# Kernel optimization log

Hardware: AMD Instinct MI355X
Metric: run time of the kernel (lower is better)

The kernel has to match this reference:

```python
import jax, jax.numpy as jnp
import numpy as np
import math

B, H, N, D = 4, 8, 2048, 64


def setup_inputs() -> dict:
    key = jax.random.key(0)
    kq, kk, kv = jax.random.split(key, 3)
    q = jax.random.normal(kq, (B, H, N, D), dtype=jnp.float32)
    k = jax.random.normal(kk, (B, H, N, D), dtype=jnp.float32)
    v = jax.random.normal(kv, (B, H, N, D), dtype=jnp.float32)
    return {"q": q, "k": k, "v": v}


def reference(q, k, v):
    # global_attention_Sub: expanded squared L2 distance ||q_i - k_j||^2
    # = qq_i - 2 q_i.k_j + kk_j, then softmax(-dist/sqrt(D)) @ v.
    scale = math.sqrt(q.shape[-1])
    inner = -2.0 * jnp.einsum('bhnd,bhmd->bhnm', q, k)          # [B,H,N,N]
    qq = jnp.sum(q * q, axis=-1, keepdims=True)                  # [B,H,N,1]
    kk = jnp.sum(k * k, axis=-1, keepdims=True)                  # [B,H,N,1]
    diff_sq = qq + inner + jnp.swapaxes(kk, -1, -2)              # [B,H,N,N]
    attn = jax.nn.softmax(-diff_sq / scale, axis=-1)
    x = jnp.einsum('bhnm,bhmd->bhnd', attn, v)                   # [B,H,N,D]
    return jnp.transpose(x, (0, 2, 1, 3))                        # [B,N,H,D]
```

## Files before the change

kernel.cpp:

```cpp
#include <hip/hip_runtime.h>

typedef __bf16 bf16x4 __attribute__((ext_vector_type(4)));
typedef __bf16 bf16x8 __attribute__((ext_vector_type(8)));
typedef float floatx4 __attribute__((ext_vector_type(4)));

constexpr int Bc = 4, Hc = 8, Nc = 2048, Dc = 64;
constexpr int BQ = 128;
constexpr int WQ = 32;
constexpr int TK = 64;
constexpr int NT = Nc / TK;
constexpr int SPS = 72;
constexpr float LOG2E = 1.44269504088896340736f;

constexpr size_t KSW_OFF = 0;
constexpr size_t VSW_OFF = (size_t)32 * NT * 8192;
constexpr size_t KKN_OFF = VSW_OFF * 2;

typedef __attribute__((address_space(1))) const unsigned int gu32;
typedef __attribute__((address_space(3))) unsigned int lu32;
__device__ __forceinline__ void dma16(const void* g, void* l) {
    __builtin_amdgcn_global_load_lds((gu32*)g, (lu32*)l, 16, 0, 0);
}
__device__ __forceinline__ void dma4(const void* g, void* l) {
    __builtin_amdgcn_global_load_lds((gu32*)g, (lu32*)l, 4, 0, 0);
}

__global__ __launch_bounds__(256) void prep_kernel(
    const float* __restrict__ Kg, const float* __restrict__ Vg, char* __restrict__ ws)
{
    __shared__ float sT[64 * 68];
    const int tid = threadIdx.x;
    const int jt = blockIdx.x, bh = blockIdx.y;

    __bf16* Ksw = (__bf16*)(ws + KSW_OFF) + ((size_t)bh * NT + jt) * 4096;
    __bf16* Vsw = (__bf16*)(ws + VSW_OFF) + ((size_t)bh * NT + jt) * 4096;
    float*  kkn = (float*)(ws + KKN_OFF) + (size_t)bh * Nc + jt * 64;
    const size_t tb = ((size_t)bh * Nc + jt * 64) * Dc;

#pragma unroll
    for (int cc = 0; cc < 2; ++cc) {
        const int g   = tid + cc * 256;
        const int key = g >> 3, kcx = g & 7;
        const int kc  = kcx ^ (key & 7);
        const float* src = Kg + tb + key * 64 + kc * 8;
        float4 a = *(const float4*)src;
        float4 b = *(const float4*)(src + 4);
        float ss = a.x*a.x + a.y*a.y + a.z*a.z + a.w*a.w
                 + b.x*b.x + b.y*b.y + b.z*b.z + b.w*b.w;
        ss += __shfl_xor(ss, 1);
        ss += __shfl_xor(ss, 2);
        ss += __shfl_xor(ss, 4);
        if (kcx == 0) kkn[key] = -(ss * 0.125f * LOG2E);
        bf16x8 c8;
        c8[0]=(__bf16)a.x; c8[1]=(__bf16)a.y; c8[2]=(__bf16)a.z; c8[3]=(__bf16)a.w;
        c8[4]=(__bf16)b.x; c8[5]=(__bf16)b.y; c8[6]=(__bf16)b.z; c8[7]=(__bf16)b.w;
        *(bf16x8*)(Ksw + g * 8) = c8;
    }

    {
        const int js = tid >> 2, dc = (tid & 3) * 16;
        const float* vr = Vg + tb + js * 64 + dc;
        float* dst = &sT[js * 68 + dc];
        *(float4*)dst       = *(const float4*)vr;
        *(float4*)(dst + 4) = *(const float4*)(vr + 4);
        *(float4*)(dst + 8) = *(const float4*)(vr + 8);
        *(float4*)(dst + 12)= *(const float4*)(vr + 12);
    }
    __syncthreads();

#pragma unroll
    for (int cc = 0; cc < 2; ++cc) {
        const int g = tid + cc * 256;
        const int d = g >> 3, kcx = g & 7;
        const int kc = kcx ^ (d & 7);
        bf16x8 c8;
#pragma unroll
        for (int e = 0; e < 8; ++e) {
            const int ee = (e + kcx) & 7;
            c8[ee] = (__bf16)sT[(kc * 8 + ee) * 68 + d];
        }
        *(bf16x8*)(Vsw + g * 8) = c8;
    }
}

__global__ __launch_bounds__(256, 2) void attn_kernel(
    const float* __restrict__ Qg, const char* __restrict__ ws, float* __restrict__ Og)
{
    __shared__ __align__(16) __bf16 sK[2][4096];
    __shared__ __align__(16) __bf16 sV[2][4096];
    __shared__ __align__(16) float  skk[2][64];
    __shared__ __align__(16) __bf16 sP[BQ * SPS];
    __shared__ __align__(16) float  sl[BQ];

    const int tid  = threadIdx.x;
    const int wave = tid >> 6;
    const int lane = tid & 63;
    const int qd   = lane >> 4;
    const int c    = lane & 15;

    const int qt = blockIdx.x;
    const int bh = blockIdx.y;

    const char* Kimg = ws + KSW_OFF + (size_t)bh * NT * 8192;
    const char* Vimg = ws + VSW_OFF + (size_t)bh * NT * 8192;
    const float* kkp = (const float*)(ws + KKN_OFF) + (size_t)bh * Nc;

    const float qscale = 0.25f * LOG2E;
    const int i0 = qt * BQ + wave * WQ;

    bf16x8 qf[2][2];
#pragma unroll
    for (int h = 0; h < 2; ++h) {
        const float* qrow = Qg + ((size_t)bh * Nc + i0 + h * 16 + c) * Dc + qd * 8;
#pragma unroll
        for (int ks = 0; ks < 2; ++ks) {
            float4 a = *(const float4*)(qrow + ks * 32);
            float4 b = *(const float4*)(qrow + ks * 32 + 4);
            bf16x8 f;
            f[0] = (__bf16)(a.x * qscale); f[1] = (__bf16)(a.y * qscale);
            f[2] = (__bf16)(a.z * qscale); f[3] = (__bf16)(a.w * qscale);
            f[4] = (__bf16)(b.x * qscale); f[5] = (__bf16)(b.y * qscale);
            f[6] = (__bf16)(b.z * qscale); f[7] = (__bf16)(b.w * qscale);
            qf[h][ks] = f;
        }
    }

    const int koff0 = c * 64 + ((qd ^ (c & 7)) << 3);
    const int koff1 = c * 64 + (((4 + qd) ^ (c & 7)) << 3);

    floatx4 oacc[2][4];
#pragma unroll
    for (int h = 0; h < 2; ++h)
#pragma unroll
        for (int dt = 0; dt < 4; ++dt)
#pragma unroll
            for (int e = 0; e < 4; ++e) oacc[h][dt][e] = 0.f;
    float lp[2] = {0.f, 0.f};

    auto stage = [&](int jt2, int b) {
        const char* ki = Kimg + (size_t)jt2 * 8192;
        const char* vi = Vimg + (size_t)jt2 * 8192;
#pragma unroll
        for (int i = 0; i < 2; ++i) {
            const int off    = wave * 2048 + i * 1024 + lane * 16;
            const int ldsoff = wave * 2048 + i * 1024;
            dma16(ki + off, (char*)&sK[b][0] + ldsoff);
            dma16(vi + off, (char*)&sV[b][0] + ldsoff);
        }
        if (wave == 3) dma4(kkp + jt2 * 64 + lane, &skk[b][0]);
    };

    stage(0, 0);

    for (int jt = 0; jt < NT; ++jt) {
        const int b = jt & 1;
        __syncthreads();
        if (jt + 1 < NT) stage(jt + 1, b ^ 1);

        floatx4 st[2][4];
#pragma unroll
        for (int kt = 0; kt < 4; ++kt) {
            floatx4 kkf = *(const floatx4*)&skk[b][kt * 16 + qd * 4];
            st[0][kt] = kkf; st[1][kt] = kkf;
        }
#pragma unroll
        for (int kt = 0; kt < 4; ++kt) {
            const __bf16* kbase = &sK[b][kt * 1024];
            bf16x8 kf0 = *(const bf16x8*)(kbase + koff0);
            bf16x8 kf1 = *(const bf16x8*)(kbase + koff1);
            st[0][kt] = __builtin_amdgcn_mfma_f32_16x16x32_bf16(kf0, qf[0][0], st[0][kt], 0, 0, 0);
            st[0][kt] = __builtin_amdgcn_mfma_f32_16x16x32_bf16(kf1, qf[0][1], st[0][kt], 0, 0, 0);
            st[1][kt] = __builtin_amdgcn_mfma_f32_16x16x32_bf16(kf0, qf[1][0], st[1][kt], 0, 0, 0);
            st[1][kt] = __builtin_amdgcn_mfma_f32_16x16x32_bf16(kf1, qf[1][1], st[1][kt], 0, 0, 0);
        }

#pragma unroll
        for (int h = 0; h < 2; ++h) {
            const int prow = wave * WQ + h * 16 + c;
#pragma unroll
            for (int kt = 0; kt < 4; ++kt) {
                float p0 = __builtin_amdgcn_exp2f(st[h][kt][0]);
                float p1 = __builtin_amdgcn_exp2f(st[h][kt][1]);
                float p2 = __builtin_amdgcn_exp2f(st[h][kt][2]);
                float p3 = __builtin_amdgcn_exp2f(st[h][kt][3]);
                lp[h] += (p0 + p1) + (p2 + p3);
                bf16x4 pk;
                pk[0] = (__bf16)p0; pk[1] = (__bf16)p1;
                pk[2] = (__bf16)p2; pk[3] = (__bf16)p3;
                *(bf16x4*)&sP[prow * SPS + kt * 16 + qd * 4] = pk;
            }
        }
        bf16x8 pf[2][2];
#pragma unroll
        for (int h = 0; h < 2; ++h)
#pragma unroll
            for (int ks = 0; ks < 2; ++ks)
                pf[h][ks] = *(const bf16x8*)&sP[(wave * WQ + h * 16 + c) * SPS + ks * 32 + qd * 8];

#pragma unroll
        for (int dt = 0; dt < 4; ++dt) {
            const __bf16* vbase = &sV[b][dt * 1024];
            bf16x8 vf0 = *(const bf16x8*)(vbase + koff0);
            bf16x8 vf1 = *(const bf16x8*)(vbase + koff1);
            oacc[0][dt] = __builtin_amdgcn_mfma_f32_16x16x32_bf16(pf[0][0], vf0, oacc[0][dt], 0, 0, 0);
            oacc[0][dt] = __builtin_amdgcn_mfma_f32_16x16x32_bf16(pf[0][1], vf1, oacc[0][dt], 0, 0, 0);
            oacc[1][dt] = __builtin_amdgcn_mfma_f32_16x16x32_bf16(pf[1][0], vf0, oacc[1][dt], 0, 0, 0);
            oacc[1][dt] = __builtin_amdgcn_mfma_f32_16x16x32_bf16(pf[1][1], vf1, oacc[1][dt], 0, 0, 0);
        }
    }

#pragma unroll
    for (int h = 0; h < 2; ++h) {
        float l = lp[h];
        l += __shfl_xor(l, 16);
        l += __shfl_xor(l, 32);
        if (qd == 0) sl[wave * WQ + h * 16 + c] = l;
    }
    const int b_ = bh >> 3, hh = bh & 7;
#pragma unroll
    for (int h = 0; h < 2; ++h) {
        floatx4 lf = *(const floatx4*)&sl[wave * WQ + h * 16 + qd * 4];
#pragma unroll
        for (int r = 0; r < 4; ++r) {
            const float inv = 1.f / lf[r];
            const int i = i0 + h * 16 + qd * 4 + r;
            float* orow = Og + (((size_t)b_ * Nc + i) * Hc + hh) * Dc + c;
#pragma unroll
            for (int dt = 0; dt < 4; ++dt)
                orow[dt * 16] = oacc[h][dt][r] * inv;
        }
    }
}

extern "C" void kernel_launch(void* const* d_in, const int* in_sizes, int n_in,
                              void* d_out, int out_size, void* d_ws, size_t ws_size,
                              hipStream_t stream) {
    const float* q = (const float*)d_in[0];
    const float* k = (const float*)d_in[1];
    const float* v = (const float*)d_in[2];
    float* out = (float*)d_out;
    char* ws = (char*)d_ws;
    prep_kernel<<<dim3(NT, Bc * Hc), 256, 0, stream>>>(k, v, ws);
    attn_kernel<<<dim3(Nc / BQ, Bc * Hc), 256, 0, stream>>>(q, ws, out);
}
```

Before: 140.8 us.

## Split key tile across wave pairs, each wave owning 64 query rows

Reorganizes the attention block so that each wave handles 64 query rows and half of each 64-key tile (a 2x2 split of query halves and key halves), instead of 32 query rows over all keys. Each K and V fragment read from LDS now feeds four MFMAs instead of two, which reduces LDS read traffic per MFMA, and the P scratch becomes per-wave with a smaller stride. In exchange, the accumulators double in register footprint (16 floatx4 for the output plus Q fragments), which may hurt occupancy at launch_bounds(256,2). It also adds a cross-wave reduction epilogue through a new LDS buffer, with extra barriers, to merge the two key-half partial outputs and row sums.

```diff
diff --git a/kernel.cpp b/kernel.cpp
--- a/kernel.cpp
+++ b/kernel.cpp
@@ -6,10 +6,9 @@
 
 constexpr int Bc = 4, Hc = 8, Nc = 2048, Dc = 64;
 constexpr int BQ = 128;
-constexpr int WQ = 32;
 constexpr int TK = 64;
 constexpr int NT = Nc / TK;
-constexpr int SPS = 72;
+constexpr int SPS = 40;
 constexpr float LOG2E = 1.44269504088896340736f;
 
 constexpr size_t KSW_OFF = 0;
@@ -56,7 +55,6 @@
         c8[4]=(__bf16)b.x; c8[5]=(__bf16)b.y; c8[6]=(__bf16)b.z; c8[7]=(__bf16)b.w;
         *(bf16x8*)(Ksw + g * 8) = c8;
     }
-
     {
         const int js = tid >> 2, dc = (tid & 3) * 16;
         const float* vr = Vg + tb + js * 64 + dc;
@@ -67,7 +65,6 @@
         *(float4*)(dst + 12)= *(const float4*)(vr + 12);
     }
     __syncthreads();
-
 #pragma unroll
     for (int cc = 0; cc < 2; ++cc) {
         const int g = tid + cc * 256;
@@ -89,14 +86,17 @@
     __shared__ __align__(16) __bf16 sK[2][4096];
     __shared__ __align__(16) __bf16 sV[2][4096];
     __shared__ __align__(16) float  skk[2][64];
-    __shared__ __align__(16) __bf16 sP[BQ * SPS];
-    __shared__ __align__(16) float  sl[BQ];
+    __shared__ __align__(16) __bf16 sP[4][64 * SPS];
+    __shared__ __align__(16) float  sl[256];
+    __shared__ __align__(16) float  sO[64 * 68];
 
     const int tid  = threadIdx.x;
     const int wave = tid >> 6;
     const int lane = tid & 63;
     const int qd   = lane >> 4;
     const int c    = lane & 15;
+    const int kh   = wave >> 1;
+    const int qh   = wave & 1;
 
     const int qt = blockIdx.x;
     const int bh = blockIdx.y;
@@ -106,12 +106,12 @@
     const float* kkp = (const float*)(ws + KKN_OFF) + (size_t)bh * Nc;
 
     const float qscale = 0.25f * LOG2E;
-    const int i0 = qt * BQ + wave * WQ;
-
-    bf16x8 qf[2][2];
-#pragma unroll
-    for (int h = 0; h < 2; ++h) {
-        const float* qrow = Qg + ((size_t)bh * Nc + i0 + h * 16 + c) * Dc + qd * 8;
+    const int i0 = qt * BQ + qh * 64;
+
+    bf16x8 qf[4][2];
+#pragma unroll
+    for (int h4 = 0; h4 < 4; ++h4) {
+        const float* qrow = Qg + ((size_t)bh * Nc + i0 + h4 * 16 + c) * Dc + qd * 8;
 #pragma unroll
         for (int ks = 0; ks < 2; ++ks) {
             float4 a = *(const float4*)(qrow + ks * 32);
@@ -121,114 +121,138 @@
             f[2] = (__bf16)(a.z * qscale); f[3] = (__bf16)(a.w * qscale);
             f[4] = (__bf16)(b.x * qscale); f[5] = (__bf16)(b.y * qscale);
             f[6] = (__bf16)(b.z * qscale); f[7] = (__bf16)(b.w * qscale);
-            qf[h][ks] = f;
-        }
-    }
-
-    const int koff0 = c * 64 + ((qd ^ (c & 7)) << 3);
-    const int koff1 = c * 64 + (((4 + qd) ^ (c & 7)) << 3);
-
-    floatx4 oacc[2][4];
-#pragma unroll
-    for (int h = 0; h < 2; ++h)
+            qf[h4][ks] = f;
+        }
+    }
+
+    int koffK[2][2], voff[4];
+#pragma unroll
+    for (int kt = 0; kt < 2; ++kt)
+#pragma unroll
+        for (int ks = 0; ks < 2; ++ks) {
+            const int key = kh * 32 + kt * 16 + c;
+            koffK[kt][ks] = key * 64 + (((ks * 4 + qd) ^ (key & 7)) << 3);
+        }
+#pragma unroll
+    for (int dt = 0; dt < 4; ++dt) {
+        const int d = dt * 16 + c;
+        voff[dt] = d * 64 + (((kh * 4 + qd) ^ (d & 7)) << 3);
+    }
+
+    floatx4 oacc[4][4];
+#pragma unroll
+    for (int h4 = 0; h4 < 4; ++h4)
 #pragma unroll
         for (int dt = 0; dt < 4; ++dt)
 #pragma unroll
-            for (int e = 0; e < 4; ++e) oacc[h][dt][e] = 0.f;
-    float lp[2] = {0.f, 0.f};
+            for (int e = 0; e < 4; ++e) oacc[h4][dt][e] = 0.f;
+    float lp[4] = {0.f, 0.f, 0.f, 0.f};
 
     auto stage = [&](int jt2, int b) {
         const char* ki = Kimg + (size_t)jt2 * 8192;
         const char* vi = Vimg + (size_t)jt2 * 8192;
 #pragma unroll
         for (int i = 0; i < 2; ++i) {
-            const int off    = wave * 2048 + i * 1024 + lane * 16;
-            const int ldsoff = wave * 2048 + i * 1024;
-            dma16(ki + off, (char*)&sK[b][0] + ldsoff);
-            dma16(vi + off, (char*)&sV[b][0] + ldsoff);
+            const int off = wave * 2048 + i * 1024;
+            dma16(ki + off + lane * 16, (char*)&sK[b][0] + off);
+            dma16(vi + off + lane * 16, (char*)&sV[b][0] + off);
         }
         if (wave == 3) dma4(kkp + jt2 * 64 + lane, &skk[b][0]);
     };
 
     stage(0, 0);
+
+    __bf16* sPw = &sP[wave][0];
 
     for (int jt = 0; jt < NT; ++jt) {
         const int b = jt & 1;
         __syncthreads();
         if (jt + 1 < NT) stage(jt + 1, b ^ 1);
 
-        floatx4 st[2][4];
-#pragma unroll
-        for (int kt = 0; kt < 4; ++kt) {
-            floatx4 kkf = *(const floatx4*)&skk[b][kt * 16 + qd * 4];
-            st[0][kt] = kkf; st[1][kt] = kkf;
-        }
-#pragma unroll
-        for (int kt = 0; kt < 4; ++kt) {
-            const __bf16* kbase = &sK[b][kt * 1024];
-            bf16x8 kf0 = *(const bf16x8*)(kbase + koff0);
-            bf16x8 kf1 = *(const bf16x8*)(kbase + koff1);
-            st[0][kt] = __builtin_amdgcn_mfma_f32_16x16x32_bf16(kf0, qf[0][0], st[0][kt], 0, 0, 0);
-            st[0][kt] = __builtin_amdgcn_mfma_f32_16x16x32_bf16(kf1, qf[0][1], st[0][kt], 0, 0, 0);
-            st[1][kt] = __builtin_amdgcn_mfma_f32_16x16x32_bf16(kf0, qf[1][0], st[1][kt], 0, 0, 0);
-            st[1][kt] = __builtin_amdgcn_mfma_f32_16x16x32_bf16(kf1, qf[1][1], st[1][kt], 0, 0, 0);
-        }
-
-#pragma unroll
-        for (int h = 0; h < 2; ++h) {
-            const int prow = wave * WQ + h * 16 + c;
-#pragma unroll
-            for (int kt = 0; kt < 4; ++kt) {
-                float p0 = __builtin_amdgcn_exp2f(st[h][kt][0]);
-                float p1 = __builtin_amdgcn_exp2f(st[h][kt][1]);
-                float p2 = __builtin_amdgcn_exp2f(st[h][kt][2]);
-                float p3 = __builtin_amdgcn_exp2f(st[h][kt][3]);
-                lp[h] += (p0 + p1) + (p2 + p3);
+#pragma unroll
+        for (int kt = 0; kt < 2; ++kt) {
+            floatx4 kkf = *(const floatx4*)&skk[b][kh * 32 + kt * 16 + qd * 4];
+            floatx4 st[4];
+#pragma unroll
+            for (int h4 = 0; h4 < 4; ++h4) st[h4] = kkf;
+#pragma unroll
+            for (int ks = 0; ks < 2; ++ks) {
+                bf16x8 kf = *(const bf16x8*)(&sK[b][0] + koffK[kt][ks]);
+                st[0] = __builtin_amdgcn_mfma_f32_16x16x32_bf16(kf, qf[0][ks], st[0], 0, 0, 0);
+                st[1] = __builtin_amdgcn_mfma_f32_16x16x32_bf16(kf, qf[1][ks], st[1], 0, 0, 0);
+                st[2] = __builtin_amdgcn_mfma_f32_16x16x32_bf16(kf, qf[2][ks], st[2], 0, 0, 0);
+                st[3] = __builtin_amdgcn_mfma_f32_16x16x32_bf16(kf, qf[3][ks], st[3], 0, 0, 0);
+            }
+#pragma unroll
+            for (int h4 = 0; h4 < 4; ++h4) {
+                float p0 = __builtin_amdgcn_exp2f(st[h4][0]);
+                float p1 = __builtin_amdgcn_exp2f(st[h4][1]);
+                float p2 = __builtin_amdgcn_exp2f(st[h4][2]);
+                float p3 = __builtin_amdgcn_exp2f(st[h4][3]);
+                lp[h4] += (p0 + p1) + (p2 + p3);
                 bf16x4 pk;
                 pk[0] = (__bf16)p0; pk[1] = (__bf16)p1;
                 pk[2] = (__bf16)p2; pk[3] = (__bf16)p3;
-                *(bf16x4*)&sP[prow * SPS + kt * 16 + qd * 4] = pk;
+                *(bf16x4*)&sPw[(h4 * 16 + c) * SPS + kt * 16 + qd * 4] = pk;
             }
         }
-        bf16x8 pf[2][2];
-#pragma unroll
-        for (int h = 0; h < 2; ++h)
-#pragma unroll
-            for (int ks = 0; ks < 2; ++ks)
-                pf[h][ks] = *(const bf16x8*)&sP[(wave * WQ + h * 16 + c) * SPS + ks * 32 + qd * 8];
+
+        bf16x8 pf[4];
+#pragma unroll
+        for (int h4 = 0; h4 < 4; ++h4)
+            pf[h4] = *(const bf16x8*)&sPw[(h4 * 16 + c) * SPS + qd * 8];
 
 #pragma unroll
         for (int dt = 0; dt < 4; ++dt) {
-            const __bf16* vbase = &sV[b][dt * 1024];
-            bf16x8 vf0 = *(const bf16x8*)(vbase + koff0);
-            bf16x8 vf1 = *(const bf16x8*)(vbase + koff1);
-            oacc[0][dt] = __builtin_amdgcn_mfma_f32_16x16x32_bf16(pf[0][0], vf0, oacc[0][dt], 0, 0, 0);
-            oacc[0][dt] = __builtin_amdgcn_mfma_f32_16x16x32_bf16(pf[0][1], vf1, oacc[0][dt], 0, 0, 0);
-            oacc[1][dt] = __builtin_amdgcn_mfma_f32_16x16x32_bf16(pf[1][0], vf0, oacc[1][dt], 0, 0, 0);
-            oacc[1][dt] = __builtin_amdgcn_mfma_f32_16x16x32_bf16(pf[1][1], vf1, oacc[1][dt], 0, 0, 0);
-        }
-    }
-
-#pragma unroll
-    for (int h = 0; h < 2; ++h) {
-        float l = lp[h];
+            bf16x8 vf = *(const bf16x8*)(&sV[b][0] + voff[dt]);
+            oacc[0][dt] = __builtin_amdgcn_mfma_f32_16x16x32_bf16(pf[0], vf, oacc[0][dt], 0, 0, 0);
+            oacc[1][dt] = __builtin_amdgcn_mfma_f32_16x16x32_bf16(pf[1], vf, oacc[1][dt], 0, 0, 0);
+            oacc[2][dt] = __builtin_amdgcn_mfma_f32_16x16x32_bf16(pf[2], vf, oacc[2][dt], 0, 0, 0);
+            oacc[3][dt] = __builtin_amdgcn_mfma_f32_16x16x32_bf16(pf[3], vf, oacc[3][dt], 0, 0, 0);
+        }
+    }
+
+#pragma unroll
+    for (int h4 = 0; h4 < 4; ++h4) {
+        float l = lp[h4];
         l += __shfl_xor(l, 16);
         l += __shfl_xor(l, 32);
-        if (qd == 0) sl[wave * WQ + h * 16 + c] = l;
-    }
+        if (qd == 0) sl[kh * 128 + qh * 64 + h4 * 16 + c] = l;
+    }
+    __syncthreads();
+
     const int b_ = bh >> 3, hh = bh & 7;
 #pragma unroll
-    for (int h = 0; h < 2; ++h) {
-        floatx4 lf = *(const floatx4*)&sl[wave * WQ + h * 16 + qd * 4];
-#pragma unroll
-        for (int r = 0; r < 4; ++r) {
-            const float inv = 1.f / lf[r];
-            const int i = i0 + h * 16 + qd * 4 + r;
-            float* orow = Og + (((size_t)b_ * Nc + i) * Hc + hh) * Dc + c;
-#pragma unroll
-            for (int dt = 0; dt < 4; ++dt)
-                orow[dt * 16] = oacc[h][dt][r] * inv;
-        }
+    for (int ph = 0; ph < 2; ++ph) {
+        if (kh == 0 && qh == ph) {
+#pragma unroll
+            for (int h4 = 0; h4 < 4; ++h4)
+#pragma unroll
+                for (int dt = 0; dt < 4; ++dt)
+#pragma unroll
+                    for (int r = 0; r < 4; ++r)
+                        sO[(h4 * 16 + qd * 4 + r) * 68 + dt * 16 + c] = oacc[h4][dt][r];
+        }
+        __syncthreads();
+        if (kh == 1 && qh == ph) {
+#pragma unroll
+            for (int h4 = 0; h4 < 4; ++h4) {
+                floatx4 l0 = *(const floatx4*)&sl[qh * 64 + h4 * 16 + qd * 4];
+                floatx4 l1 = *(const floatx4*)&sl[128 + qh * 64 + h4 * 16 + qd * 4];
+#pragma unroll
+                for (int r = 0; r < 4; ++r) {
+                    const float inv = 1.f / (l0[r] + l1[r]);
+                    const int i = i0 + h4 * 16 + qd * 4 + r;
+                    float* orow = Og + (((size_t)b_ * Nc + i) * Hc + hh) * Dc + c;
+#pragma unroll
+                    for (int dt = 0; dt < 4; ++dt) {
+                        const float part = sO[(h4 * 16 + qd * 4 + r) * 68 + dt * 16 + c];
+                        orow[dt * 16] = (oacc[h4][dt][r] + part) * inv;
+                    }
+                }
+            }
+        }
+        __syncthreads();
     }
 }
 
```

Measured after the change: 144.4 us. +2.5%, slower.

## Halve query tile per block to 64 rows and raise occupancy

Applied to the files above, without the earlier changes.

Each wave now handles 16 query rows instead of 32, so a block covers 64 queries and the grid doubles to 1024 blocks. The launch bound is raised to 3 blocks per SM and the exp/store of P is interleaved per key subtile. The goal is more parallel blocks and more resident waves to hide latency. The cost is twice as much K/V tile loading per query, and each K/V fragment read from LDS now feeds half as many MFMAs.

```diff
diff --git a/kernel.cpp b/kernel.cpp
--- a/kernel.cpp
+++ b/kernel.cpp
@@ -5,8 +5,8 @@
 typedef float floatx4 __attribute__((ext_vector_type(4)));
 
 constexpr int Bc = 4, Hc = 8, Nc = 2048, Dc = 64;
-constexpr int BQ = 128;
-constexpr int WQ = 32;
+constexpr int BQ = 64;
+constexpr int WQ = 16;
 constexpr int TK = 64;
 constexpr int NT = Nc / TK;
 constexpr int SPS = 72;
@@ -56,7 +56,6 @@
         c8[4]=(__bf16)b.x; c8[5]=(__bf16)b.y; c8[6]=(__bf16)b.z; c8[7]=(__bf16)b.w;
         *(bf16x8*)(Ksw + g * 8) = c8;
     }
-
     {
         const int js = tid >> 2, dc = (tid & 3) * 16;
         const float* vr = Vg + tb + js * 64 + dc;
@@ -67,7 +66,6 @@
         *(float4*)(dst + 12)= *(const float4*)(vr + 12);
     }
     __syncthreads();
-
 #pragma unroll
     for (int cc = 0; cc < 2; ++cc) {
         const int g = tid + cc * 256;
@@ -83,13 +81,13 @@
     }
 }
 
-__global__ __launch_bounds__(256, 2) void attn_kernel(
+__global__ __launch_bounds__(256, 3) void attn_kernel(
     const float* __restrict__ Qg, const char* __restrict__ ws, float* __restrict__ Og)
 {
     __shared__ __align__(16) __bf16 sK[2][4096];
     __shared__ __align__(16) __bf16 sV[2][4096];
     __shared__ __align__(16) float  skk[2][64];
-    __shared__ __align__(16) __bf16 sP[BQ * SPS];
+    __shared__ __align__(16) __bf16 sP[4 * WQ * SPS];
     __shared__ __align__(16) float  sl[BQ];
 
     const int tid  = threadIdx.x;
@@ -106,12 +104,11 @@
     const float* kkp = (const float*)(ws + KKN_OFF) + (size_t)bh * Nc;
 
     const float qscale = 0.25f * LOG2E;
-    const int i0 = qt * BQ + wave * WQ;
-
-    bf16x8 qf[2][2];
-#pragma unroll
-    for (int h = 0; h < 2; ++h) {
-        const float* qrow = Qg + ((size_t)bh * Nc + i0 + h * 16 + c) * Dc + qd * 8;
+    const int i0w = qt * BQ + wave * WQ;
+
+    bf16x8 qf[2];
+    {
+        const float* qrow = Qg + ((size_t)bh * Nc + i0w + c) * Dc + qd * 8;
 #pragma unroll
         for (int ks = 0; ks < 2; ++ks) {
             float4 a = *(const float4*)(qrow + ks * 32);
@@ -121,114 +118,89 @@
             f[2] = (__bf16)(a.z * qscale); f[3] = (__bf16)(a.w * qscale);
             f[4] = (__bf16)(b.x * qscale); f[5] = (__bf16)(b.y * qscale);
             f[6] = (__bf16)(b.z * qscale); f[7] = (__bf16)(b.w * qscale);
-            qf[h][ks] = f;
+            qf[ks] = f;
         }
     }
 
     const int koff0 = c * 64 + ((qd ^ (c & 7)) << 3);
     const int koff1 = c * 64 + (((4 + qd) ^ (c & 7)) << 3);
 
-    floatx4 oacc[2][4];
-#pragma unroll
-    for (int h = 0; h < 2; ++h)
-#pragma unroll
-        for (int dt = 0; dt < 4; ++dt)
-#pragma unroll
-            for (int e = 0; e < 4; ++e) oacc[h][dt][e] = 0.f;
-    float lp[2] = {0.f, 0.f};
+    floatx4 oacc[4];
+#pragma unroll
+    for (int dt = 0; dt < 4; ++dt)
+#pragma unroll
+        for (int e = 0; e < 4; ++e) oacc[dt][e] = 0.f;
+    float lp = 0.f;
 
     auto stage = [&](int jt2, int b) {
         const char* ki = Kimg + (size_t)jt2 * 8192;
         const char* vi = Vimg + (size_t)jt2 * 8192;
 #pragma unroll
         for (int i = 0; i < 2; ++i) {
-            const int off    = wave * 2048 + i * 1024 + lane * 16;
-            const int ldsoff = wave * 2048 + i * 1024;
-            dma16(ki + off, (char*)&sK[b][0] + ldsoff);
-            dma16(vi + off, (char*)&sV[b][0] + ldsoff);
+            const int off = wave * 2048 + i * 1024;
+            dma16(ki + off + lane * 16, (char*)&sK[b][0] + off);
+            dma16(vi + off + lane * 16, (char*)&sV[b][0] + off);
         }
         if (wave == 3) dma4(kkp + jt2 * 64 + lane, &skk[b][0]);
     };
 
     stage(0, 0);
+
+    __bf16* sPw = &sP[wave * WQ * SPS];
 
     for (int jt = 0; jt < NT; ++jt) {
         const int b = jt & 1;
         __syncthreads();
         if (jt + 1 < NT) stage(jt + 1, b ^ 1);
 
-        floatx4 st[2][4];
 #pragma unroll
         for (int kt = 0; kt < 4; ++kt) {
-            floatx4 kkf = *(const floatx4*)&skk[b][kt * 16 + qd * 4];
-            st[0][kt] = kkf; st[1][kt] = kkf;
-        }
-#pragma unroll
-        for (int kt = 0; kt < 4; ++kt) {
+            floatx4 st = *(const floatx4*)&skk[b][kt * 16 + qd * 4];
             const __bf16* kbase = &sK[b][kt * 1024];
             bf16x8 kf0 = *(const bf16x8*)(kbase + koff0);
             bf16x8 kf1 = *(const bf16x8*)(kbase + koff1);
-            st[0][kt] = __builtin_amdgcn_mfma_f32_16x16x32_bf16(kf0, qf[0][0], st[0][kt], 0, 0, 0);
-            st[0][kt] = __builtin_amdgcn_mfma_f32_16x16x32_bf16(kf1, qf[0][1], st[0][kt], 0, 0, 0);
-            st[1][kt] = __builtin_amdgcn_mfma_f32_16x16x32_bf16(kf0, qf[1][0], st[1][kt], 0, 0, 0);
-            st[1][kt] = __builtin_amdgcn_mfma_f32_16x16x32_bf16(kf1, qf[1][1], st[1][kt], 0, 0, 0);
-        }
-
-#pragma unroll
-        for (int h = 0; h < 2; ++h) {
-            const int prow = wave * WQ + h * 16 + c;
-#pragma unroll
-            for (int kt = 0; kt < 4; ++kt) {
-                float p0 = __builtin_amdgcn_exp2f(st[h][kt][0]);
-                float p1 = __builtin_amdgcn_exp2f(st[h][kt][1]);
-                float p2 = __builtin_amdgcn_exp2f(st[h][kt][2]);
-                float p3 = __builtin_amdgcn_exp2f(st[h][kt][3]);
-                lp[h] += (p0 + p1) + (p2 + p3);
-                bf16x4 pk;
-                pk[0] = (__bf16)p0; pk[1] = (__bf16)p1;
-                pk[2] = (__bf16)p2; pk[3] = (__bf16)p3;
-                *(bf16x4*)&sP[prow * SPS + kt * 16 + qd * 4] = pk;
-            }
-        }
-        bf16x8 pf[2][2];
-#pragma unroll
-        for (int h = 0; h < 2; ++h)
-#pragma unroll
-            for (int ks = 0; ks < 2; ++ks)
-                pf[h][ks] = *(const bf16x8*)&sP[(wave * WQ + h * 16 + c) * SPS + ks * 32 + qd * 8];
+            st = __builtin_amdgcn_mfma_f32_16x16x32_bf16(kf0, qf[0], st, 0, 0, 0);
+            st = __builtin_amdgcn_mfma_f32_16x16x32_bf16(kf1, qf[1], st, 0, 0, 0);
+            float p0 = __builtin_amdgcn_exp2f(st[0]);
+            float p1 = __builtin_amdgcn_exp2f(st[1]);
+            float p2 = __builtin_amdgcn_exp2f(st[2]);
+            float p3 = __builtin_amdgcn_exp2f(st[3]);
+            lp += (p0 + p1) + (p2 + p3);
+            bf16x4 pk;
+            pk[0] = (__bf16)p0; pk[1] = (__bf16)p1;
+            pk[2] = (__bf16)p2; pk[3] = (__bf16)p3;
+            *(bf16x4*)&sPw[c * SPS + kt * 16 + qd * 4] = pk;
+        }
+
+        bf16x8 pf0 = *(const bf16x8*)&sPw[c * SPS + qd * 8];
+        bf16x8 pf1 = *(const bf16x8*)&sPw[c * SPS + 32 + qd * 8];
 
 #pragma unroll
         for (int dt = 0; dt < 4; ++dt) {
             const __bf16* vbase = &sV[b][dt * 1024];
             bf16x8 vf0 = *(const bf16x8*)(vbase + koff0);
             bf16x8 vf1 = *(const bf16x8*)(vbase + koff1);
-            oacc[0][dt] = __builtin_amdgcn_mfma_f32_16x16x32_bf16(pf[0][0], vf0, oacc[0][dt], 0, 0, 0);
-            oacc[0][dt] = __builtin_amdgcn_mfma_f32_16x16x32_bf16(pf[0][1], vf1, oacc[0][dt], 0, 0, 0);
-            oacc[1][dt] = __builtin_amdgcn_mfma_f32_16x16x32_bf16(pf[1][0], vf0, oacc[1][dt], 0, 0, 0);
-            oacc[1][dt] = __builtin_amdgcn_mfma_f32_16x16x32_bf16(pf[1][1], vf1, oacc[1][dt], 0, 0, 0);
-        }
-    }
-
-#pragma unroll
-    for (int h = 0; h < 2; ++h) {
-        float l = lp[h];
+            oacc[dt] = __builtin_amdgcn_mfma_f32_16x16x32_bf16(pf0, vf0, oacc[dt], 0, 0, 0);
+            oacc[dt] = __builtin_amdgcn_mfma_f32_16x16x32_bf16(pf1, vf1, oacc[dt], 0, 0, 0);
+        }
+    }
+
+    {
+        float l = lp;
         l += __shfl_xor(l, 16);
         l += __shfl_xor(l, 32);
-        if (qd == 0) sl[wave * WQ + h * 16 + c] = l;
+        if (qd == 0) sl[wave * WQ + c] = l;
     }
     const int b_ = bh >> 3, hh = bh & 7;
-#pragma unroll
-    for (int h = 0; h < 2; ++h) {
-        floatx4 lf = *(const floatx4*)&sl[wave * WQ + h * 16 + qd * 4];
-#pragma unroll
-        for (int r = 0; r < 4; ++r) {
-            const float inv = 1.f / lf[r];
-            const int i = i0 + h * 16 + qd * 4 + r;
-            float* orow = Og + (((size_t)b_ * Nc + i) * Hc + hh) * Dc + c;
-#pragma unroll
-            for (int dt = 0; dt < 4; ++dt)
-                orow[dt * 16] = oacc[h][dt][r] * inv;
-        }
+    floatx4 lf = *(const floatx4*)&sl[wave * WQ + qd * 4];
+#pragma unroll
+    for (int r = 0; r < 4; ++r) {
+        const float inv = 1.f / lf[r];
+        const int i = i0w + qd * 4 + r;
+        float* orow = Og + (((size_t)b_ * Nc + i) * Hc + hh) * Dc + c;
+#pragma unroll
+        for (int dt = 0; dt < 4; ++dt)
+            orow[dt * 16] = oacc[dt][r] * inv;
     }
 }
 
```

Measured after the change: 152.9 us. 1.09x slower.

## Split key range across two blocks with atomic-ticket partial merge

Applied to the files above, without the earlier changes.

Splits each query tile's key loop across two blocks along grid z, each writing unnormalized partial outputs and row sums to workspace. An atomic ticket lets the second-finishing block merge both partials and write the normalized output. The intent is more blocks for better CU occupancy and latency hiding, at the cost of partial-buffer global traffic, an extra memset, and fences. It is enabled only if the workspace is large enough.

```diff
diff --git a/kernel.cpp b/kernel.cpp
--- a/kernel.cpp
+++ b/kernel.cpp
@@ -12,9 +12,13 @@
 constexpr int SPS = 72;
 constexpr float LOG2E = 1.44269504088896340736f;
 
-constexpr size_t KSW_OFF = 0;
-constexpr size_t VSW_OFF = (size_t)32 * NT * 8192;
-constexpr size_t KKN_OFF = VSW_OFF * 2;
+constexpr size_t KSW_OFF    = 0;
+constexpr size_t VSW_OFF    = (size_t)32 * NT * 8192;
+constexpr size_t KKN_OFF    = VSW_OFF * 2;
+constexpr size_t TICKET_OFF = (size_t)17 * 1024 * 1024;
+constexpr size_t PART_OFF   = TICKET_OFF + 4096;
+constexpr size_t PART_STRIDE = 33280;
+constexpr size_t WS_NEED    = PART_OFF + (size_t)1024 * PART_STRIDE;
 
 typedef __attribute__((address_space(1))) const unsigned int gu32;
 typedef __attribute__((address_space(3))) unsigned int lu32;
@@ -56,7 +60,6 @@
         c8[4]=(__bf16)b.x; c8[5]=(__bf16)b.y; c8[6]=(__bf16)b.z; c8[7]=(__bf16)b.w;
         *(bf16x8*)(Ksw + g * 8) = c8;
     }
-
     {
         const int js = tid >> 2, dc = (tid & 3) * 16;
         const float* vr = Vg + tb + js * 64 + dc;
@@ -67,7 +70,6 @@
         *(float4*)(dst + 12)= *(const float4*)(vr + 12);
     }
     __syncthreads();
-
 #pragma unroll
     for (int cc = 0; cc < 2; ++cc) {
         const int g = tid + cc * 256;
@@ -84,13 +86,15 @@
 }
 
 __global__ __launch_bounds__(256, 2) void attn_kernel(
-    const float* __restrict__ Qg, const char* __restrict__ ws, float* __restrict__ Og)
+    const float* __restrict__ Qg, char* __restrict__ ws, float* __restrict__ Og,
+    const int split)
 {
     __shared__ __align__(16) __bf16 sK[2][4096];
     __shared__ __align__(16) __bf16 sV[2][4096];
     __shared__ __align__(16) float  skk[2][64];
     __shared__ __align__(16) __bf16 sP[BQ * SPS];
     __shared__ __align__(16) float  sl[BQ];
+    __shared__ int sflag;
 
     const int tid  = threadIdx.x;
     const int wave = tid >> 6;
@@ -100,6 +104,7 @@
 
     const int qt = blockIdx.x;
     const int bh = blockIdx.y;
+    const int kh = blockIdx.z;
 
     const char* Kimg = ws + KSW_OFF + (size_t)bh * NT * 8192;
     const char* Vimg = ws + VSW_OFF + (size_t)bh * NT * 8192;
@@ -150,12 +155,14 @@
         if (wave == 3) dma4(kkp + jt2 * 64 + lane, &skk[b][0]);
     };
 
-    stage(0, 0);
-
-    for (int jt = 0; jt < NT; ++jt) {
-        const int b = jt & 1;
+    const int nth = NT / split;
+    const int jt0 = kh * nth;
+    stage(jt0, 0);
+
+    for (int it = 0; it < nth; ++it) {
+        const int b = it & 1;
         __syncthreads();
-        if (jt + 1 < NT) stage(jt + 1, b ^ 1);
+        if (it + 1 < nth) stage(jt0 + it + 1, b ^ 1);
 
         floatx4 st[2][4];
 #pragma unroll
@@ -209,25 +216,71 @@
         }
     }
 
+    float lred[2];
 #pragma unroll
     for (int h = 0; h < 2; ++h) {
         float l = lp[h];
         l += __shfl_xor(l, 16);
         l += __shfl_xor(l, 32);
+        lred[h] = l;
         if (qd == 0) sl[wave * WQ + h * 16 + c] = l;
     }
     const int b_ = bh >> 3, hh = bh & 7;
-#pragma unroll
-    for (int h = 0; h < 2; ++h) {
-        floatx4 lf = *(const floatx4*)&sl[wave * WQ + h * 16 + qd * 4];
-#pragma unroll
-        for (int r = 0; r < 4; ++r) {
-            const float inv = 1.f / lf[r];
-            const int i = i0 + h * 16 + qd * 4 + r;
-            float* orow = Og + (((size_t)b_ * Nc + i) * Hc + hh) * Dc + c;
-#pragma unroll
-            for (int dt = 0; dt < 4; ++dt)
-                orow[dt * 16] = oacc[h][dt][r] * inv;
+
+    if (split == 1) {
+#pragma unroll
+        for (int h = 0; h < 2; ++h) {
+            floatx4 lf = *(const floatx4*)&sl[wave * WQ + h * 16 + qd * 4];
+#pragma unroll
+            for (int r = 0; r < 4; ++r) {
+                const float inv = 1.f / lf[r];
+                const int i = i0 + h * 16 + qd * 4 + r;
+                float* orow = Og + (((size_t)b_ * Nc + i) * Hc + hh) * Dc + c;
+#pragma unroll
+                for (int dt = 0; dt < 4; ++dt)
+                    orow[dt * 16] = oacc[h][dt][r] * inv;
+            }
+        }
+    } else {
+        const int pidx = bh * 16 + qt;
+        const int pid  = pidx * 2 + kh;
+        float* mypart = (float*)(ws + PART_OFF + (size_t)pid * PART_STRIDE);
+#pragma unroll
+        for (int h = 0; h < 2; ++h)
+#pragma unroll
+            for (int r = 0; r < 4; ++r) {
+                const int row = wave * WQ + h * 16 + qd * 4 + r;
+#pragma unroll
+                for (int dt = 0; dt < 4; ++dt)
+                    mypart[row * 64 + dt * 16 + c] = oacc[h][dt][r];
+            }
+        if (qd == 0) {
+#pragma unroll
+            for (int h = 0; h < 2; ++h)
+                mypart[8192 + wave * WQ + h * 16 + c] = lred[h];
+        }
+        __threadfence();
+        if (tid == 0)
+            sflag = (int)atomicAdd((unsigned int*)(ws + TICKET_OFF) + pidx, 1u);
+        __syncthreads();
+        if (sflag == 1) {
+            __threadfence();
+            const float* op = (const float*)(ws + PART_OFF + (size_t)(pid ^ 1) * PART_STRIDE);
+#pragma unroll
+            for (int h = 0; h < 2; ++h) {
+                floatx4 lf  = *(const floatx4*)&sl[wave * WQ + h * 16 + qd * 4];
+                floatx4 lpf = *(const floatx4*)&op[8192 + wave * WQ + h * 16 + qd * 4];
+#pragma unroll
+                for (int r = 0; r < 4; ++r) {
+                    const float inv = 1.f / (lf[r] + lpf[r]);
+                    const int row = wave * WQ + h * 16 + qd * 4 + r;
+                    const int i = qt * BQ + row;
+                    float* orow = Og + (((size_t)b_ * Nc + i) * Hc + hh) * Dc + c;
+#pragma unroll
+                    for (int dt = 0; dt < 4; ++dt)
+                        orow[dt * 16] = (oacc[h][dt][r] + op[row * 64 + dt * 16 + c]) * inv;
+                }
+            }
         }
     }
 }
@@ -240,6 +293,9 @@
     const float* v = (const float*)d_in[2];
     float* out = (float*)d_out;
     char* ws = (char*)d_ws;
+    const int split = (ws_size >= WS_NEED) ? 2 : 1;
+    if (split == 2)
+        hipMemsetAsync(ws + TICKET_OFF, 0, 4096, stream);
     prep_kernel<<<dim3(NT, Bc * Hc), 256, 0, stream>>>(k, v, ws);
-    attn_kernel<<<dim3(Nc / BQ, Bc * Hc), 256, 0, stream>>>(q, ws, out);
-}
+    attn_kernel<<<dim3(Nc / BQ, Bc * Hc, split), 256, 0, stream>>>(q, ws, out, split);
+}
```

Result: slower. 327.6 us (+132.7%).
